# Kernel tuning notes

Hardware: AMD Instinct MI355X
Metric: run time of the kernel (lower is better)

Reference implementation:

```python
import jax, jax.numpy as jnp
import numpy as np

EPS = 1e-5  # torch BatchNorm2d default


def _conv1x1(x, w):
    # x: [n, cin, h, w], w: [cout, cin] (1x1 conv == per-pixel matmul)
    return jnp.einsum('nchw,oc->nohw', x, w)


def _bn(x, gamma, beta, mean, var):
    # inference-mode BatchNorm2d over channel dim
    scale = gamma * jax.lax.rsqrt(var + EPS)
    shift = beta - mean * scale
    return x * scale[None, :, None, None] + shift[None, :, None, None]


def setup_inputs() -> dict:
    key = jax.random.key(0)
    ks = jax.random.split(key, 24)
    n, c, h, w = 16, 256, 64, 64
    width, planes = c // 2, c
    inp = {
        'x': jax.random.normal(ks[0], (n, c, h, w), jnp.float32),
        'w_theta': jax.random.normal(ks[1], (width, c), jnp.float32) * 0.05,
        'w_phi': jax.random.normal(ks[2], (width, c), jnp.float32) * 0.05,
        'w_g': jax.random.normal(ks[3], (width, c), jnp.float32) * 0.05,
        'w_zeta': jax.random.normal(ks[4], (planes, width), jnp.float32) * 0.05,
    }
    for i, (name, dim) in enumerate([('bn1', width), ('bn2', width), ('bn3', width), ('bn4', planes)]):
        k = 5 + 4 * i
        inp[f'{name}_gamma'] = jax.random.uniform(ks[k], (dim,), jnp.float32, 0.5, 1.5)
        inp[f'{name}_beta'] = jax.random.normal(ks[k + 1], (dim,), jnp.float32) * 0.1
        inp[f'{name}_mean'] = jax.random.normal(ks[k + 2], (dim,), jnp.float32) * 0.1
        inp[f'{name}_var'] = jax.random.uniform(ks[k + 3], (dim,), jnp.float32, 0.5, 1.5)
    return inp


def reference(x, w_theta, w_phi, w_g, w_zeta,
              bn1_gamma, bn1_beta, bn1_mean, bn1_var,
              bn2_gamma, bn2_beta, bn2_mean, bn2_var,
              bn3_gamma, bn3_beta, bn3_mean, bn3_var,
              bn4_gamma, bn4_beta, bn4_mean, bn4_var):
    n, c, h, w = x.shape
    theta = jax.nn.relu(_bn(_conv1x1(x, w_theta), bn1_gamma, bn1_beta, bn1_mean, bn1_var))
    phi = jax.nn.relu(_bn(_conv1x1(x, w_phi), bn2_gamma, bn2_beta, bn2_mean, bn2_var))
    g = jax.nn.relu(_bn(_conv1x1(x, w_g), bn3_gamma, bn3_beta, bn3_mean, bn3_var))

    width = theta.shape[1]
    hw = h * w
    theta = theta.reshape(n, width, hw)  # [n, C', S]
    phi = phi.reshape(n, width, hw)      # [n, C', S]
    g = g.reshape(n, width, hw)          # [n, C', S]

    # (theta^T @ phi) @ g^T == theta^T @ (phi @ g^T): no softmax, so associativity
    # lets us contract over pixels first -> O(S*C'^2) instead of O(S^2*C').
    kv = jnp.einsum('ncs,nds->ncd', phi, g)      # [n, C', C']
    out = jnp.einsum('ncs,ncd->nsd', theta, kv)  # [n, S, C']

    # faithful to torch: reshape (not transpose) [n, S, C'] -> [n, C', h, w]
    out = out.reshape(n, width, h, w)
    out = _bn(_conv1x1(out, w_zeta), bn4_gamma, bn4_beta, bn4_mean, bn4_var)
    return jax.nn.relu(out + x)
```

## Files before the change

kernel.cpp:

```cpp
#include <hip/hip_runtime.h>

#define BN_EPS 1e-5f

typedef unsigned short u16;
typedef __bf16 bf16x8 __attribute__((ext_vector_type(8)));
typedef float floatx4 __attribute__((ext_vector_type(4)));
typedef u16 u16x4 __attribute__((ext_vector_type(4)));
typedef u16 u16x8 __attribute__((ext_vector_type(8)));

__device__ __forceinline__ u16 f2bf(float f) {
    union { float f; unsigned int u; } v; v.f = f;
    unsigned int r = (v.u + 0x7fffu + ((v.u >> 16) & 1u)) >> 16;
    return (u16)r;
}

__device__ __forceinline__ float bf2f(u16 b) {
    union { unsigned int u; float f; } v; v.u = ((unsigned int)b) << 16;
    return v.f;
}

__device__ __forceinline__ unsigned int cvtpk(float lo, float hi) {
    unsigned int r;
    asm("v_cvt_pk_bf16_f32 %0, %1, %2" : "=v"(r) : "v"(lo), "v"(hi));
    return r;
}

__device__ __forceinline__ void gld16(const void* gsrc, void* ldst) {
    __builtin_amdgcn_global_load_lds(
        (const __attribute__((address_space(1))) unsigned int*)gsrc,
        (__attribute__((address_space(3))) unsigned int*)ldst, 16, 0, 0);
}

__device__ __forceinline__ int addsw(int seg, int s) {
    return (seg + (s & 7) + ((s >> 3) & 7)) & 7;
}

__global__ __launch_bounds__(256) void prep_kernel(
    const float* __restrict__ wt, const float* __restrict__ wp,
    const float* __restrict__ wg, const float* __restrict__ wz,
    const float* __restrict__ g1, const float* __restrict__ b1,
    const float* __restrict__ m1, const float* __restrict__ v1,
    const float* __restrict__ g2, const float* __restrict__ b2,
    const float* __restrict__ m2, const float* __restrict__ v2,
    const float* __restrict__ g3, const float* __restrict__ b3,
    const float* __restrict__ m3, const float* __restrict__ v3,
    const float* __restrict__ g4, const float* __restrict__ b4,
    const float* __restrict__ m4, const float* __restrict__ v4,
    u16* __restrict__ W1bf, float* __restrict__ shift1,
    u16* __restrict__ Wzbf, float* __restrict__ shift4)
{
    int id = blockIdx.x * 256 + threadIdx.x;
    if (id < 384 * 256) {
        int r = id >> 8, c = id & 255;
        int grp = r >> 7, ch = r & 127;
        const float* wsrc = grp == 0 ? wt : (grp == 1 ? wp : wg);
        const float* gg = grp == 0 ? g1 : (grp == 1 ? g2 : g3);
        const float* bb = grp == 0 ? b1 : (grp == 1 ? b2 : b3);
        const float* mm = grp == 0 ? m1 : (grp == 1 ? m2 : m3);
        const float* vv = grp == 0 ? v1 : (grp == 1 ? v2 : v3);
        float scale = gg[ch] * rsqrtf(vv[ch] + BN_EPS);
        W1bf[id] = f2bf(wsrc[ch * 256 + c] * scale);
        if (c == 0) shift1[r] = bb[ch] - mm[ch] * scale;
    }
    if (id < 256 * 128) {
        int o = id >> 7;
        float scale = g4[o] * rsqrtf(v4[o] + BN_EPS);
        Wzbf[id] = f2bf(wz[id] * scale);
        if ((id & 127) == 0) shift4[o] = b4[o] - m4[o] * scale;
    }
}

__global__ __launch_bounds__(512, 2) void k1_kernel(
    const float* __restrict__ x, const u16* __restrict__ W1,
    const float* __restrict__ shift1,
    u16* __restrict__ theta_sm, u16* __restrict__ partials)
{
    const int sk = blockIdx.x, n = blockIdx.y;
    const int tid = threadIdx.x;
    const int w = tid >> 6, lane = tid & 63;
    const int quad = lane >> 4, l16 = lane & 15;

    __shared__ __align__(16) u16 pool[32768];
    u16* B0 = pool;
    u16* B1 = pool + 8192;

    floatx4 acc[3][8];
#pragma unroll
    for (int i = 0; i < 3; ++i)
#pragma unroll
        for (int j = 0; j < 8; ++j) acc[i][j] = floatx4{0.f, 0.f, 0.f, 0.f};

    const int cp = w * 4 + quad;
    const float* xb = x + ((size_t)n * 256 + 2 * cp) * 4096 + sk * 128;

    float4 xv[2][2];

    auto loadx = [&](int kc) {
#pragma unroll
        for (int ch = 0; ch < 2; ++ch)
#pragma unroll
            for (int hb = 0; hb < 2; ++hb)
                xv[ch][hb] = *((const float4*)(xb + (size_t)(kc * 64 + ch) * 4096) + hb * 16 + l16);
    };
    auto writeB = [&](u16* B) {
        unsigned int* bd = (unsigned int*)B;
#pragma unroll
        for (int hb = 0; hb < 2; ++hb)
#pragma unroll
            for (int j = 0; j < 4; ++j) {
                int s = hb * 64 + l16 * 4 + j;
                bd[s * 32 + addsw(w, s) * 4 + quad] =
                    cvtpk(((const float*)&xv[0][hb])[j], ((const float*)&xv[1][hb])[j]);
            }
    };
    auto compute = [&](int kc, const u16* B) {
#pragma unroll
        for (int kk = 0; kk < 2; ++kk) {
            bf16x8 a[3];
#pragma unroll
            for (int mt = 0; mt < 3; ++mt) {
                a[mt] = *(const bf16x8*)(W1 + (size_t)(mt * 128 + w * 16 + l16) * 256
                                             + kc * 64 + (kk * 4 + quad) * 8);
            }
#pragma unroll
            for (int ni = 0; ni < 8; ++ni) {
                int s = ni * 16 + l16;
                int phys = addsw(kk * 4 + quad, s);
                bf16x8 b = *(const bf16x8*)(B + s * 64 + phys * 8);
#pragma unroll
                for (int mt = 0; mt < 3; ++mt)
                    acc[mt][ni] = __builtin_amdgcn_mfma_f32_16x16x32_bf16(
                        a[mt], b, acc[mt][ni], 0, 0, 0);
            }
        }
    };

    loadx(0);
    writeB(B0);
    loadx(1);
    __syncthreads();
    writeB(B1);
    loadx(2);
    compute(0, B0);
    __syncthreads();
    writeB(B0);
    loadx(3);
    compute(1, B1);
    __syncthreads();
    writeB(B1);
    compute(2, B0);
    __syncthreads();
    compute(3, B1);
    __syncthreads();

    const int ocq = w * 16 + quad * 4;
    {
        float sh0 = shift1[ocq + 0], sh1 = shift1[ocq + 1];
        float sh2 = shift1[ocq + 2], sh3 = shift1[ocq + 3];
#pragma unroll
        for (int ni = 0; ni < 8; ++ni) {
            int s = sk * 128 + ni * 16 + l16;
            float v0 = acc[0][ni][0] + sh0, v1 = acc[0][ni][1] + sh1;
            float v2 = acc[0][ni][2] + sh2, v3 = acc[0][ni][3] + sh3;
            v0 = v0 > 0.f ? v0 : 0.f;
            v1 = v1 > 0.f ? v1 : 0.f;
            v2 = v2 > 0.f ? v2 : 0.f;
            v3 = v3 > 0.f ? v3 : 0.f;
            uint2 pk;
            pk.x = cvtpk(v0, v1);
            pk.y = cvtpk(v2, v3);
            *(uint2*)(theta_sm + (size_t)n * 524288 + (size_t)s * 128 + ocq) = pk;
        }
    }
#pragma unroll
    for (int mt = 1; mt < 3; ++mt)
#pragma unroll
        for (int r = 0; r < 4; ++r) {
            int ch = ocq + r;
            float sh = shift1[mt * 128 + ch];
#pragma unroll
            for (int ni = 0; ni < 8; ++ni) {
                int sl = ni * 16 + l16;
                int half = sl >> 6, s6 = sl & 63;
                int phys = (s6 >> 3) ^ (ch & 7);
                float val = acc[mt][ni][r] + sh;
                val = val > 0.f ? val : 0.f;
                pool[((mt - 1) * 2 + half) * 8192 + ch * 64 + phys * 8 + (s6 & 7)] = f2bf(val);
            }
        }
    __syncthreads();

    floatx4 kv[8];
#pragma unroll
    for (int i = 0; i < 8; ++i) kv[i] = floatx4{0.f, 0.f, 0.f, 0.f};
#pragma unroll
    for (int h = 0; h < 2; ++h)
#pragma unroll
        for (int kk = 0; kk < 2; ++kk) {
            int rd = w * 16 + l16;
            int physa = (kk * 4 + quad) ^ (rd & 7);
            bf16x8 a = *(const bf16x8*)(pool + (2 + h) * 8192 + rd * 64 + physa * 8);
#pragma unroll
            for (int ci = 0; ci < 8; ++ci) {
                int rc = ci * 16 + l16;
                int physb = (kk * 4 + quad) ^ (rc & 7);
                bf16x8 b = *(const bf16x8*)(pool + h * 8192 + rc * 64 + physb * 8);
                kv[ci] = __builtin_amdgcn_mfma_f32_16x16x32_bf16(a, b, kv[ci], 0, 0, 0);
            }
        }

    u16* outp = partials + (size_t)(n * 32 + sk) * 16384;
#pragma unroll
    for (int r = 0; r < 4; ++r) {
        int d = w * 16 + quad * 4 + r;
#pragma unroll
        for (int ci = 0; ci < 8; ++ci)
            outp[d * 128 + ci * 16 + l16] = f2bf(kv[ci][r]);
    }
}

__global__ __launch_bounds__(256) void kv_reduce_kernel(
    const u16* __restrict__ partials, u16* __restrict__ kvT)
{
    int n = blockIdx.y;
    int f4 = blockIdx.x * 256 + threadIdx.x;
    float s0 = 0.f, s1 = 0.f, s2 = 0.f, s3 = 0.f;
#pragma unroll
    for (int kc = 0; kc < 32; ++kc) {
        u16x4 v = *(const u16x4*)(partials + (size_t)(n * 32 + kc) * 16384 + f4 * 4);
        s0 += bf2f(v[0]); s1 += bf2f(v[1]); s2 += bf2f(v[2]); s3 += bf2f(v[3]);
    }
    u16x4 o; o[0] = f2bf(s0); o[1] = f2bf(s1); o[2] = f2bf(s2); o[3] = f2bf(s3);
    *(u16x4*)(kvT + (size_t)n * 16384 + f4 * 4) = o;
}

__global__ __launch_bounds__(512, 2) void k34_kernel(
    const u16* __restrict__ theta_sm, const u16* __restrict__ kvT,
    const u16* __restrict__ Wz, const float* __restrict__ shift4,
    const float* __restrict__ x, float* __restrict__ out)
{
    const int st = blockIdx.x, n = blockIdx.y;
    const int tid = threadIdx.x;
    const int w = tid >> 6, lane = tid & 63;
    const int quad = lane >> 4, l16 = lane & 15;

    __shared__ __align__(16) u16 pool[32768];
    u16* Y = pool + 16384;

    const u16* tbase = theta_sm + (size_t)n * 524288 + (size_t)st * 128;
    const u16* kbase = kvT + (size_t)n * 16384;

    floatx4 acc3[8];
#pragma unroll
    for (int i = 0; i < 8; ++i) acc3[i] = floatx4{0.f, 0.f, 0.f, 0.f};

    auto stageTK = [&](u16* T, u16* K, int ch) {
#pragma unroll
        for (int i = 0; i < 2; ++i) {
            int op = w * 2 + i;
            int r = op * 8 + (lane >> 3);
            int lseg = (lane & 7) ^ (r & 7);
            gld16(tbase + (size_t)r * 4096 + ch * 64 + lseg * 8, T + op * 512);
            gld16(kbase + (size_t)r * 128 + ch * 64 + lseg * 8, K + op * 512);
        }
    };
    auto stageWz = [&](int ch) {
#pragma unroll
        for (int i = 0; i < 4; ++i) {
            int op = w * 4 + i;
            int r = op * 8 + (lane >> 3);
            int lseg = (lane & 7) ^ (r & 7);
            gld16(Wz + (size_t)r * 128 + ch * 64 + lseg * 8, pool + op * 512);
        }
    };
    auto comp3 = [&](const u16* T, const u16* K) {
#pragma unroll
        for (int kk = 0; kk < 2; ++kk) {
            int rc2 = w * 16 + l16;
            int physa = (kk * 4 + quad) ^ (rc2 & 7);
            bf16x8 a = *(const bf16x8*)(T + rc2 * 64 + physa * 8);
#pragma unroll
            for (int di = 0; di < 8; ++di) {
                int rd = di * 16 + l16;
                int physb = (kk * 4 + quad) ^ (rd & 7);
                bf16x8 b = *(const bf16x8*)(K + rd * 64 + physb * 8);
                acc3[di] = __builtin_amdgcn_mfma_f32_16x16x32_bf16(a, b, acc3[di], 0, 0, 0);
            }
        }
    };

    stageTK(pool, pool + 8192, 0);
    __syncthreads();
    stageTK(pool + 16384, pool + 24576, 1);
    comp3(pool, pool + 8192);
    __syncthreads();
    stageWz(0);
    comp3(pool + 16384, pool + 24576);
    __syncthreads();

#pragma unroll
    for (int di = 0; di < 8; ++di) {
        int j = di * 16 + l16;
#pragma unroll
        for (int r = 0; r < 4; ++r) {
            int c2 = w * 16 + quad * 4 + r;
            int half = c2 >> 6, c64 = c2 & 63;
            int phys = (c64 >> 3) ^ (j & 7);
            Y[half * 8192 + j * 64 + phys * 8 + (c64 & 7)] = f2bf(acc3[di][r]);
        }
    }
    __syncthreads();

    floatx4 acc4[2][8];
#pragma unroll
    for (int i = 0; i < 2; ++i)
#pragma unroll
        for (int j = 0; j < 8; ++j) acc4[i][j] = floatx4{0.f, 0.f, 0.f, 0.f};

    auto comp4 = [&](int ch) {
#pragma unroll
        for (int kk = 0; kk < 2; ++kk) {
            bf16x8 a[2];
#pragma unroll
            for (int mi = 0; mi < 2; ++mi) {
                int r = w * 32 + mi * 16 + l16;
                int phys = (kk * 4 + quad) ^ (r & 7);
                a[mi] = *(const bf16x8*)(pool + r * 64 + phys * 8);
            }
#pragma unroll
            for (int ni = 0; ni < 8; ++ni) {
                int s = ni * 16 + l16;
                int phys = (kk * 4 + quad) ^ (s & 7);
                bf16x8 b = *(const bf16x8*)(Y + ch * 8192 + s * 64 + phys * 8);
#pragma unroll
                for (int mi = 0; mi < 2; ++mi)
                    acc4[mi][ni] = __builtin_amdgcn_mfma_f32_16x16x32_bf16(
                        a[mi], b, acc4[mi][ni], 0, 0, 0);
            }
        }
    };

    comp4(0);
    __syncthreads();
    stageWz(1);
    __syncthreads();
    comp4(1);

#pragma unroll
    for (int mi = 0; mi < 2; ++mi)
#pragma unroll
        for (int r = 0; r < 4; ++r) {
            int o = w * 32 + mi * 16 + quad * 4 + r;
            float sh = shift4[o];
#pragma unroll
            for (int ni = 0; ni < 8; ++ni) {
                int s2 = st * 128 + ni * 16 + l16;
                size_t idx = ((size_t)n * 256 + o) * 4096 + s2;
                float val = acc4[mi][ni][r] + sh + x[idx];
                out[idx] = val > 0.f ? val : 0.f;
            }
        }
}

extern "C" void kernel_launch(void* const* d_in, const int* in_sizes, int n_in,
                              void* d_out, int out_size, void* d_ws, size_t ws_size,
                              hipStream_t stream)
{
    const float* x  = (const float*)d_in[0];
    const float* wt = (const float*)d_in[1];
    const float* wp = (const float*)d_in[2];
    const float* wg = (const float*)d_in[3];
    const float* wz = (const float*)d_in[4];
    const float* bn[16];
    for (int i = 0; i < 16; ++i) bn[i] = (const float*)d_in[5 + i];

    char* ws = (char*)d_ws;
    u16*   W1bf     = (u16*)  (ws + 0);
    float* shift1   = (float*)(ws + 196608);
    u16*   Wzbf     = (u16*)  (ws + 198144);
    float* shift4   = (float*)(ws + 263680);
    u16*   theta_sm = (u16*)  (ws + 264704);
    u16*   partials = (u16*)  (ws + 17041920);
    u16*   kvT      = (u16*)  (ws + 33819136);
    float* out = (float*)d_out;

    prep_kernel<<<384, 256, 0, stream>>>(
        wt, wp, wg, wz,
        bn[0], bn[1], bn[2], bn[3],
        bn[4], bn[5], bn[6], bn[7],
        bn[8], bn[9], bn[10], bn[11],
        bn[12], bn[13], bn[14], bn[15],
        W1bf, shift1, Wzbf, shift4);

    k1_kernel<<<dim3(32, 16), 512, 0, stream>>>(x, W1bf, shift1, theta_sm, partials);
    kv_reduce_kernel<<<dim3(16, 16), 256, 0, stream>>>(partials, kvT);
    k34_kernel<<<dim3(32, 16), 512, 0, stream>>>(theta_sm, kvT, Wzbf, shift4, x, out);
}
```

Before: 196.8 us.

## Pre-transpose x to pixel-major bf16 and stage k1 tiles via global_load_lds

Adds a separate transpose kernel that converts x from channel-major fp32 to pixel-major bf16 in workspace. k1 then stages its B tiles with direct global-to-LDS 16-byte loads and a simple XOR swizzle, instead of loading fp32 into registers, converting and scattering into LDS. This is meant to cut register pressure and LDS write overhead in k1. In exchange it adds a full extra pass over x (a 64MB fp32 read and a 32MB bf16 write) plus one more kernel launch.

Measured after the change: 213.3 us. +8.4%, slower.

```diff
diff --git a/kernel.cpp b/kernel.cpp
--- a/kernel.cpp
+++ b/kernel.cpp
@@ -29,10 +29,6 @@
     __builtin_amdgcn_global_load_lds(
         (const __attribute__((address_space(1))) unsigned int*)gsrc,
         (__attribute__((address_space(3))) unsigned int*)ldst, 16, 0, 0);
-}
-
-__device__ __forceinline__ int addsw(int seg, int s) {
-    return (seg + (s & 7) + ((s >> 3) & 7)) & 7;
 }
 
 __global__ __launch_bounds__(256) void prep_kernel(
@@ -70,8 +66,41 @@
     }
 }
 
+__global__ __launch_bounds__(256) void xpose_kernel(
+    const float* __restrict__ x, u16* __restrict__ xT)
+{
+    const int st = blockIdx.x, ct = blockIdx.y, n = blockIdx.z;
+    const int tid = threadIdx.x;
+    __shared__ float tile[64][65];
+
+    const float* xb = x + ((size_t)n * 256 + ct * 64) * 4096 + st * 64;
+    {
+        int c = tid >> 2, s4 = tid & 3;
+#pragma unroll
+        for (int j = 0; j < 4; ++j) {
+            float4 v = *((const float4*)(xb + (size_t)c * 4096) + s4 * 4 + j);
+            int s = (s4 * 4 + j) * 4;
+            tile[c][s + 0] = v.x; tile[c][s + 1] = v.y;
+            tile[c][s + 2] = v.z; tile[c][s + 3] = v.w;
+        }
+    }
+    __syncthreads();
+    {
+        int s = tid >> 2, cq = tid & 3;
+        unsigned int o[8];
+#pragma unroll
+        for (int p = 0; p < 8; ++p)
+            o[p] = cvtpk(tile[cq * 16 + 2 * p][s], tile[cq * 16 + 2 * p + 1][s]);
+        u16* dst = xT + ((size_t)n * 4096 + st * 64 + s) * 256 + ct * 64 + cq * 16;
+        uint4 w0 = {o[0], o[1], o[2], o[3]};
+        uint4 w1 = {o[4], o[5], o[6], o[7]};
+        *(uint4*)dst = w0;
+        *(uint4*)(dst + 8) = w1;
+    }
+}
+
 __global__ __launch_bounds__(512, 2) void k1_kernel(
-    const float* __restrict__ x, const u16* __restrict__ W1,
+    const u16* __restrict__ xT, const u16* __restrict__ W1,
     const float* __restrict__ shift1,
     u16* __restrict__ theta_sm, u16* __restrict__ partials)
 {
@@ -90,28 +119,16 @@
 #pragma unroll
         for (int j = 0; j < 8; ++j) acc[i][j] = floatx4{0.f, 0.f, 0.f, 0.f};
 
-    const int cp = w * 4 + quad;
-    const float* xb = x + ((size_t)n * 256 + 2 * cp) * 4096 + sk * 128;
-
-    float4 xv[2][2];
-
-    auto loadx = [&](int kc) {
-#pragma unroll
-        for (int ch = 0; ch < 2; ++ch)
-#pragma unroll
-            for (int hb = 0; hb < 2; ++hb)
-                xv[ch][hb] = *((const float4*)(xb + (size_t)(kc * 64 + ch) * 4096) + hb * 16 + l16);
-    };
-    auto writeB = [&](u16* B) {
-        unsigned int* bd = (unsigned int*)B;
-#pragma unroll
-        for (int hb = 0; hb < 2; ++hb)
-#pragma unroll
-            for (int j = 0; j < 4; ++j) {
-                int s = hb * 64 + l16 * 4 + j;
-                bd[s * 32 + addsw(w, s) * 4 + quad] =
-                    cvtpk(((const float*)&xv[0][hb])[j], ((const float*)&xv[1][hb])[j]);
-            }
+    const u16* xTb = xT + (size_t)n * 1048576 + (size_t)sk * 128 * 256;
+
+    auto stageB = [&](u16* B, int kc) {
+#pragma unroll
+        for (int i = 0; i < 2; ++i) {
+            int op = w * 2 + i;
+            int r = op * 8 + (lane >> 3);
+            int lseg = (lane & 7) ^ (r & 7);
+            gld16(xTb + (size_t)r * 256 + kc * 64 + lseg * 8, B + op * 512);
+        }
     };
     auto compute = [&](int kc, const u16* B) {
 #pragma unroll
@@ -125,7 +142,7 @@
 #pragma unroll
             for (int ni = 0; ni < 8; ++ni) {
                 int s = ni * 16 + l16;
-                int phys = addsw(kk * 4 + quad, s);
+                int phys = (kk * 4 + quad) ^ (s & 7);
                 bf16x8 b = *(const bf16x8*)(B + s * 64 + phys * 8);
 #pragma unroll
                 for (int mt = 0; mt < 3; ++mt)
@@ -135,19 +152,15 @@
         }
     };
 
-    loadx(0);
-    writeB(B0);
-    loadx(1);
-    __syncthreads();
-    writeB(B1);
-    loadx(2);
+    stageB(B0, 0);
+    __syncthreads();
+    stageB(B1, 1);
     compute(0, B0);
     __syncthreads();
-    writeB(B0);
-    loadx(3);
+    stageB(B0, 2);
     compute(1, B1);
     __syncthreads();
-    writeB(B1);
+    stageB(B1, 3);
     compute(2, B0);
     __syncthreads();
     compute(3, B1);
@@ -382,6 +395,7 @@
     u16*   theta_sm = (u16*)  (ws + 264704);
     u16*   partials = (u16*)  (ws + 17041920);
     u16*   kvT      = (u16*)  (ws + 33819136);
+    u16*   xT       = (u16*)  (ws + 34343424);
     float* out = (float*)d_out;
 
     prep_kernel<<<384, 256, 0, stream>>>(
@@ -392,7 +406,8 @@
         bn[12], bn[13], bn[14], bn[15],
         W1bf, shift1, Wzbf, shift4);
 
-    k1_kernel<<<dim3(32, 16), 512, 0, stream>>>(x, W1bf, shift1, theta_sm, partials);
+    xpose_kernel<<<dim3(64, 4, 16), 256, 0, stream>>>(x, xT);
+    k1_kernel<<<dim3(32, 16), 512, 0, stream>>>(xT, W1bf, shift1, theta_sm, partials);
     kv_reduce_kernel<<<dim3(16, 16), 256, 0, stream>>>(partials, kvT);
     k34_kernel<<<dim3(32, 16), 512, 0, stream>>>(theta_sm, kvT, Wzbf, shift4, x, out);
 }
```

## Halve k1 pixel tile to 64, load whole K slab at once, double grid

Applied to the files above, without the earlier changes.

The k1 kernel now handles 64 pixels per block instead of 128, launching 1024 blocks instead of 512. Each block loads its full 256-channel x slab into LDS in one pass with a new XOR swizzle, replacing the software double-buffered 4-stage pipeline. LDS per block and accumulator count are halved, and launch bounds allow 3 blocks per CU, aiming for more occupancy and parallelism. In exchange the kv partials double (64 per image), so the reduce kernel reads twice as much data, and there is no longer any overlap between loads and MFMA inside a block.

Result: slower. 217.8 us (+10.7%).

```diff
diff --git a/kernel.cpp b/kernel.cpp
--- a/kernel.cpp
+++ b/kernel.cpp
@@ -29,10 +29,6 @@
     __builtin_amdgcn_global_load_lds(
         (const __attribute__((address_space(1))) unsigned int*)gsrc,
         (__attribute__((address_space(3))) unsigned int*)ldst, 16, 0, 0);
-}
-
-__device__ __forceinline__ int addsw(int seg, int s) {
-    return (seg + (s & 7) + ((s >> 3) & 7)) & 7;
 }
 
 __global__ __launch_bounds__(256) void prep_kernel(
@@ -70,7 +66,7 @@
     }
 }
 
-__global__ __launch_bounds__(512, 2) void k1_kernel(
+__global__ __launch_bounds__(512, 3) void k1_kernel(
     const float* __restrict__ x, const u16* __restrict__ W1,
     const float* __restrict__ shift1,
     u16* __restrict__ theta_sm, u16* __restrict__ partials)
@@ -80,77 +76,61 @@
     const int w = tid >> 6, lane = tid & 63;
     const int quad = lane >> 4, l16 = lane & 15;
 
-    __shared__ __align__(16) u16 pool[32768];
-    u16* B0 = pool;
-    u16* B1 = pool + 8192;
-
-    floatx4 acc[3][8];
+    __shared__ __align__(16) u16 pool[16384];
+    unsigned int* Bdw = (unsigned int*)pool;
+
+    {
+        const int cp = tid >> 2;
+        const int sq = tid & 3;
+        const float* r0 = x + ((size_t)n * 256 + 2 * cp) * 4096 + sk * 64 + sq * 16;
+        float4 v0[4], v1[4];
+#pragma unroll
+        for (int j = 0; j < 4; ++j) {
+            v0[j] = *((const float4*)r0 + j);
+            v1[j] = *((const float4*)(r0 + 4096) + j);
+        }
+        const int seg_hi = (cp >> 2) & 24;
+        const int seg_lo = (cp >> 2) & 7;
+        const int dwin = cp & 3;
+#pragma unroll
+        for (int j = 0; j < 4; ++j)
+#pragma unroll
+            for (int e = 0; e < 4; ++e) {
+                int s = sq * 16 + j * 4 + e;
+                int phys = seg_hi | (seg_lo ^ (s & 7));
+                Bdw[s * 128 + phys * 4 + dwin] =
+                    cvtpk(((const float*)&v0[j])[e], ((const float*)&v1[j])[e]);
+            }
+    }
+
+    floatx4 acc[3][4];
 #pragma unroll
     for (int i = 0; i < 3; ++i)
 #pragma unroll
-        for (int j = 0; j < 8; ++j) acc[i][j] = floatx4{0.f, 0.f, 0.f, 0.f};
-
-    const int cp = w * 4 + quad;
-    const float* xb = x + ((size_t)n * 256 + 2 * cp) * 4096 + sk * 128;
-
-    float4 xv[2][2];
-
-    auto loadx = [&](int kc) {
-#pragma unroll
-        for (int ch = 0; ch < 2; ++ch)
-#pragma unroll
-            for (int hb = 0; hb < 2; ++hb)
-                xv[ch][hb] = *((const float4*)(xb + (size_t)(kc * 64 + ch) * 4096) + hb * 16 + l16);
-    };
-    auto writeB = [&](u16* B) {
-        unsigned int* bd = (unsigned int*)B;
-#pragma unroll
-        for (int hb = 0; hb < 2; ++hb)
-#pragma unroll
-            for (int j = 0; j < 4; ++j) {
-                int s = hb * 64 + l16 * 4 + j;
-                bd[s * 32 + addsw(w, s) * 4 + quad] =
-                    cvtpk(((const float*)&xv[0][hb])[j], ((const float*)&xv[1][hb])[j]);
-            }
-    };
-    auto compute = [&](int kc, const u16* B) {
+        for (int j = 0; j < 4; ++j) acc[i][j] = floatx4{0.f, 0.f, 0.f, 0.f};
+
+    __syncthreads();
+
+#pragma unroll
+    for (int kc = 0; kc < 4; ++kc)
 #pragma unroll
         for (int kk = 0; kk < 2; ++kk) {
             bf16x8 a[3];
 #pragma unroll
-            for (int mt = 0; mt < 3; ++mt) {
+            for (int mt = 0; mt < 3; ++mt)
                 a[mt] = *(const bf16x8*)(W1 + (size_t)(mt * 128 + w * 16 + l16) * 256
                                              + kc * 64 + (kk * 4 + quad) * 8);
-            }
-#pragma unroll
-            for (int ni = 0; ni < 8; ++ni) {
+#pragma unroll
+            for (int ni = 0; ni < 4; ++ni) {
                 int s = ni * 16 + l16;
-                int phys = addsw(kk * 4 + quad, s);
-                bf16x8 b = *(const bf16x8*)(B + s * 64 + phys * 8);
+                int phys = kc * 8 + ((kk * 4 + quad) ^ (s & 7));
+                bf16x8 b = *(const bf16x8*)(pool + s * 256 + phys * 8);
 #pragma unroll
                 for (int mt = 0; mt < 3; ++mt)
                     acc[mt][ni] = __builtin_amdgcn_mfma_f32_16x16x32_bf16(
                         a[mt], b, acc[mt][ni], 0, 0, 0);
             }
         }
-    };
-
-    loadx(0);
-    writeB(B0);
-    loadx(1);
-    __syncthreads();
-    writeB(B1);
-    loadx(2);
-    compute(0, B0);
-    __syncthreads();
-    writeB(B0);
-    loadx(3);
-    compute(1, B1);
-    __syncthreads();
-    writeB(B1);
-    compute(2, B0);
-    __syncthreads();
-    compute(3, B1);
     __syncthreads();
 
     const int ocq = w * 16 + quad * 4;
@@ -158,8 +138,8 @@
         float sh0 = shift1[ocq + 0], sh1 = shift1[ocq + 1];
         float sh2 = shift1[ocq + 2], sh3 = shift1[ocq + 3];
 #pragma unroll
-        for (int ni = 0; ni < 8; ++ni) {
-            int s = sk * 128 + ni * 16 + l16;
+        for (int ni = 0; ni < 4; ++ni) {
+            int s = sk * 64 + ni * 16 + l16;
             float v0 = acc[0][ni][0] + sh0, v1 = acc[0][ni][1] + sh1;
             float v2 = acc[0][ni][2] + sh2, v3 = acc[0][ni][3] + sh3;
             v0 = v0 > 0.f ? v0 : 0.f;
@@ -179,13 +159,12 @@
             int ch = ocq + r;
             float sh = shift1[mt * 128 + ch];
 #pragma unroll
-            for (int ni = 0; ni < 8; ++ni) {
+            for (int ni = 0; ni < 4; ++ni) {
                 int sl = ni * 16 + l16;
-                int half = sl >> 6, s6 = sl & 63;
-                int phys = (s6 >> 3) ^ (ch & 7);
+                int phys = (sl >> 3) ^ (ch & 7);
                 float val = acc[mt][ni][r] + sh;
                 val = val > 0.f ? val : 0.f;
-                pool[((mt - 1) * 2 + half) * 8192 + ch * 64 + phys * 8 + (s6 & 7)] = f2bf(val);
+                pool[(mt - 1) * 8192 + ch * 64 + phys * 8 + (sl & 7)] = f2bf(val);
             }
         }
     __syncthreads();
@@ -194,22 +173,20 @@
 #pragma unroll
     for (int i = 0; i < 8; ++i) kv[i] = floatx4{0.f, 0.f, 0.f, 0.f};
 #pragma unroll
-    for (int h = 0; h < 2; ++h)
-#pragma unroll
-        for (int kk = 0; kk < 2; ++kk) {
-            int rd = w * 16 + l16;
-            int physa = (kk * 4 + quad) ^ (rd & 7);
-            bf16x8 a = *(const bf16x8*)(pool + (2 + h) * 8192 + rd * 64 + physa * 8);
-#pragma unroll
-            for (int ci = 0; ci < 8; ++ci) {
-                int rc = ci * 16 + l16;
-                int physb = (kk * 4 + quad) ^ (rc & 7);
-                bf16x8 b = *(const bf16x8*)(pool + h * 8192 + rc * 64 + physb * 8);
-                kv[ci] = __builtin_amdgcn_mfma_f32_16x16x32_bf16(a, b, kv[ci], 0, 0, 0);
-            }
-        }
-
-    u16* outp = partials + (size_t)(n * 32 + sk) * 16384;
+    for (int kk = 0; kk < 2; ++kk) {
+        int rd = w * 16 + l16;
+        int physa = (kk * 4 + quad) ^ (rd & 7);
+        bf16x8 a = *(const bf16x8*)(pool + 8192 + rd * 64 + physa * 8);
+#pragma unroll
+        for (int ci = 0; ci < 8; ++ci) {
+            int rc = ci * 16 + l16;
+            int physb = (kk * 4 + quad) ^ (rc & 7);
+            bf16x8 b = *(const bf16x8*)(pool + rc * 64 + physb * 8);
+            kv[ci] = __builtin_amdgcn_mfma_f32_16x16x32_bf16(a, b, kv[ci], 0, 0, 0);
+        }
+    }
+
+    u16* outp = partials + (size_t)(n * 64 + sk) * 16384;
 #pragma unroll
     for (int r = 0; r < 4; ++r) {
         int d = w * 16 + quad * 4 + r;
@@ -226,8 +203,8 @@
     int f4 = blockIdx.x * 256 + threadIdx.x;
     float s0 = 0.f, s1 = 0.f, s2 = 0.f, s3 = 0.f;
 #pragma unroll
-    for (int kc = 0; kc < 32; ++kc) {
-        u16x4 v = *(const u16x4*)(partials + (size_t)(n * 32 + kc) * 16384 + f4 * 4);
+    for (int kc = 0; kc < 64; ++kc) {
+        u16x4 v = *(const u16x4*)(partials + (size_t)(n * 64 + kc) * 16384 + f4 * 4);
         s0 += bf2f(v[0]); s1 += bf2f(v[1]); s2 += bf2f(v[2]); s3 += bf2f(v[3]);
     }
     u16x4 o; o[0] = f2bf(s0); o[1] = f2bf(s1); o[2] = f2bf(s2); o[3] = f2bf(s3);
@@ -381,7 +358,7 @@
     float* shift4   = (float*)(ws + 263680);
     u16*   theta_sm = (u16*)  (ws + 264704);
     u16*   partials = (u16*)  (ws + 17041920);
-    u16*   kvT      = (u16*)  (ws + 33819136);
+    u16*   kvT      = (u16*)  (ws + 50596352);
     float* out = (float*)d_out;
 
     prep_kernel<<<384, 256, 0, stream>>>(
@@ -392,7 +369,7 @@
         bn[12], bn[13], bn[14], bn[15],
         W1bf, shift1, Wzbf, shift4);
 
-    k1_kernel<<<dim3(32, 16), 512, 0, stream>>>(x, W1bf, shift1, theta_sm, partials);
+    k1_kernel<<<dim3(64, 16), 512, 0, stream>>>(x, W1bf, shift1, theta_sm, partials);
     kv_reduce_kernel<<<dim3(16, 16), 256, 0, stream>>>(partials, kvT);
     k34_kernel<<<dim3(32, 16), 512, 0, stream>>>(theta_sm, kvT, Wzbf, shift4, x, out);
 }
```
